# Optimization experiments

Measured on AMD Instinct MI355X. Metric: run time of the kernel, lower is better.

The kernel has to match this reference:

```python
import jax, jax.numpy as jnp
import numpy as np
from jax import lax

B, T, C, F_IN = 16, 128, 64, 128
H, FO = 4, 16          # GAT heads, out-features per head (gat_out)
HID = 32               # LSTM hidden (bidirectional -> 64)
NCLS = 3
TOPK, THR, TEMP = 2, 0.3, 1.5


def _layernorm(x, g, b, eps=1e-5):
    m = x.mean(-1, keepdims=True)
    v = ((x - m) ** 2).mean(-1, keepdims=True)
    return (x - m) / jnp.sqrt(v + eps) * g + b


def setup_inputs() -> dict:
    key = jax.random.key(0)
    ks = jax.random.split(key, 16)
    def lin(k, o, i):
        return jax.random.normal(k, (o, i), jnp.float32) / np.sqrt(i)
    return {
        "x": jax.random.uniform(ks[0], (B, T, C, F_IN), jnp.float32),
        "spec_w": jnp.ones((C, F_IN), jnp.float32),
        "gat_W": lin(ks[1], H * FO, F_IN),
        "gat_a": jax.random.normal(ks[2], (H, 2 * FO), jnp.float32),
        "gat_norm_g": jnp.ones((H * FO,), jnp.float32),
        "gat_norm_b": jnp.zeros((H * FO,), jnp.float32),
        "gat_res_W": lin(ks[3], H * FO, F_IN),
        "gat_res_b": jnp.zeros((H * FO,), jnp.float32),
        "lW_ih_f": lin(ks[4], 4 * HID, H * FO),
        "lW_hh_f": lin(ks[5], 4 * HID, HID),
        "lb_ih_f": jnp.zeros((4 * HID,), jnp.float32),
        "lb_hh_f": jnp.zeros((4 * HID,), jnp.float32),
        "lW_ih_b": lin(ks[6], 4 * HID, H * FO),
        "lW_hh_b": lin(ks[7], 4 * HID, HID),
        "lb_ih_b": jnp.zeros((4 * HID,), jnp.float32),
        "lb_hh_b": jnp.zeros((4 * HID,), jnp.float32),
        "ta_W": lin(ks[8], 2 * HID, 2 * HID),
        "ta_b": jnp.zeros((2 * HID,), jnp.float32),
        "ta_v": lin(ks[9], 1, 2 * HID),
        "cp_W": lin(ks[10], 1, 2 * HID),
        "cp_b": jnp.zeros((1,), jnp.float32),
        "norm_g": jnp.ones((2 * HID,), jnp.float32),
        "norm_b": jnp.zeros((2 * HID,), jnp.float32),
        "fc1_W": lin(ks[11], 32, 2 * HID),
        "fc1_b": jnp.zeros((32,), jnp.float32),
        "fc2_W": lin(ks[12], NCLS, 32),
        "fc2_b": jnp.zeros((NCLS,), jnp.float32),
    }


def _lstm(xs, Wih, Whh, bih, bhh):
    # xs: [T, N, in] -> [T, N, HID]; PyTorch gate order i,f,g,o
    N = xs.shape[1]
    def step(carry, xt):
        h, c = carry
        z = xt @ Wih.T + h @ Whh.T + bih + bhh
        i, f, g, o = jnp.split(z, 4, axis=-1)
        c = jax.nn.sigmoid(f) * c + jax.nn.sigmoid(i) * jnp.tanh(g)
        h = jax.nn.sigmoid(o) * jnp.tanh(c)
        return (h, c), h
    init = (jnp.zeros((N, HID), xs.dtype), jnp.zeros((N, HID), xs.dtype))
    return lax.scan(step, init, xs)[1]


def reference(x, spec_w, gat_W, gat_a, gat_norm_g, gat_norm_b, gat_res_W, gat_res_b,
              lW_ih_f, lW_hh_f, lb_ih_f, lb_hh_f, lW_ih_b, lW_hh_b, lb_ih_b, lb_hh_b,
              ta_W, ta_b, ta_v, cp_W, cp_b, norm_g, norm_b,
              fc1_W, fc1_b, fc2_W, fc2_b):
    # --- spectral weighting ---
    x = x * jax.nn.sigmoid(spec_w)                               # [B,T,C,F]
    # --- per-sample correlation graph (vectorized over B,T) ---
    Hn = x / (jnp.linalg.norm(x, axis=-1, keepdims=True) + 1e-8)
    A = jnp.einsum('btcf,btdf->bcd', Hn, Hn) / T                 # mean over T
    A = 0.5 * (A + jnp.swapaxes(A, 1, 2))
    # --- sparsify: per-row top-(k+1), threshold, off-diagonal, symmetrize ---
    _, idx = lax.top_k(A, TOPK + 1)                              # [B,C,k+1]
    topm = jax.nn.one_hot(idx, C).sum(axis=2) > 0                # [B,C,C]
    eye = jnp.eye(C, dtype=bool)
    keep = topm & (A > THR) & ~eye
    keep = keep | jnp.swapaxes(keep, 1, 2)
    A_s = jnp.where(keep, A, 0.0)                                # [B,C,C]
    # --- multi-head GAT, vectorized over all timesteps ---
    Wh = jnp.einsum('btcf,gf->btcg', x, gat_W).reshape(B, T, C, H, FO)
    ei = jnp.einsum('btchf,hf->btch', Wh, gat_a[:, :FO])
    ej = jnp.einsum('btchf,hf->btch', Wh, gat_a[:, FO:])
    e = ei[:, :, :, None, :] + ej[:, :, None, :, :]              # [B,T,C,C,H]
    e = jnp.where(e > 0, e, 0.2 * e)                             # LeakyReLU(0.2)
    mask = (A_s > 0) | eye                                       # [B,C,C]
    e = jnp.where(mask[:, None, :, :, None], e, -1e9)
    An = A_s / (A_s.sum(-1, keepdims=True) + 1e-8)
    e = e + An[:, None, :, :, None]
    alpha = jax.nn.softmax(e / TEMP, axis=3)                     # over j
    Hout = jnp.einsum('btijh,btjhf->btihf', alpha, Wh).reshape(B, T, C, H * FO)
    res = jnp.einsum('btcf,gf->btcg', x, gat_res_W) + gat_res_b
    g = jax.nn.relu(_layernorm(Hout + res, gat_norm_g, gat_norm_b))  # [B,T,C,64]
    # --- BiLSTM over T for each (faithful torch .view on [B,T,C,Fp]) ---
    seq = g.reshape(B * C, T, H * FO)
    xs = jnp.swapaxes(seq, 0, 1)                                 # [T,N,64]
    hf = _lstm(xs, lW_ih_f, lW_hh_f, lb_ih_f, lb_hh_f)
    hb = _lstm(xs[::-1], lW_ih_b, lW_hh_b, lb_ih_b, lb_hh_b)[::-1]
    h = jnp.swapaxes(jnp.concatenate([hf, hb], -1), 0, 1)        # [N,T,64]
    # --- temporal attention ---
    sc = (jnp.tanh(h @ ta_W.T + ta_b) @ ta_v.T)[..., 0]          # [N,T]
    al = jax.nn.softmax(sc / TEMP, axis=1)
    hp = (h * al[..., None]).sum(1)                              # [N,64]
    # --- channel attention pooling ---
    xc = hp.reshape(B, C, 2 * HID)
    w = jax.nn.softmax(xc @ cp_W.T + cp_b, axis=1)               # [B,C,1]
    pooled = (xc * w).sum(1)                                     # [B,64]
    pooled = _layernorm(pooled, norm_g, norm_b)
    hid = jax.nn.relu(pooled @ fc1_W.T + fc1_b)
    return hid @ fc2_W.T + fc2_b                                 # [B,3]
```

## Files before the change

### kernel.cpp

```cpp
#include <hip/hip_runtime.h>
#include <math.h>

#define BB 16
#define TT 128
#define CC 64
#define FF 128

static constexpr float INV_TEMP = 1.0f / 1.5f;

static constexpr size_t OFF_WTT   = 8192;
static constexpr size_t OFF_RTT   = 16384;
static constexpr size_t OFF_TAWT  = 24576;
static constexpr size_t OFF_AN    = 28672;
static constexpr size_t OFF_A     = 94208;
static constexpr size_t OFF_G     = 1208320;
static constexpr size_t OFF_H     = 9596928;
static constexpr size_t OFF_HP    = 17985536;
static constexpr size_t OFF_WIHT  = 18051072;
static constexpr size_t OFF_ZX    = 18067456;
static constexpr size_t OFF_XW    = OFF_ZX;
static constexpr size_t OFF_WHS   = OFF_ZX + 16777216;
static constexpr size_t OFF_RS    = OFF_ZX + 25165824;
static constexpr size_t OFF_APART = OFF_WHS;

__global__ __launch_bounds__(256) void k_xw(const float* __restrict__ x,
                                            const float* __restrict__ spec_w,
                                            float* __restrict__ xw) {
    const size_t i4 = (size_t)blockIdx.x * 256 + threadIdx.x;
    const float4 xv = ((const float4*)x)[i4];
    const int cf = (int)((i4 * 4) & 8191);
    const float4 wv = *(const float4*)(spec_w + cf);
    float4 o;
    o.x = xv.x / (1.f + __expf(-wv.x));
    o.y = xv.y / (1.f + __expf(-wv.y));
    o.z = xv.z / (1.f + __expf(-wv.z));
    o.w = xv.w / (1.f + __expf(-wv.w));
    ((float4*)xw)[i4] = o;
}

__global__ __launch_bounds__(256) void k_prep(const float* __restrict__ gat_W,
                                              const float* __restrict__ gat_rW,
                                              const float* __restrict__ ta_W,
                                              const float* __restrict__ Wihf,
                                              const float* __restrict__ Wihb,
                                              float* __restrict__ ws) {
    int i = blockIdx.x * 256 + threadIdx.x;
    if (i < 8192) {
        int k = i >> 6, g = i & 63;
        ws[OFF_WTT + i] = gat_W[g * 128 + k];
    } else if (i < 16384) {
        int j = i - 8192; int k = j >> 6, g = j & 63;
        ws[OFF_RTT + j] = gat_rW[g * 128 + k];
    } else if (i < 20480) {
        int j = i - 16384; int v = j >> 6, u = j & 63;
        ws[OFF_TAWT + j] = ta_W[u * 64 + v];
    } else if (i < 36864) {
        int j = i - 20480;
        int dir = j >> 13, rem = j & 8191, k = rem >> 7, gg = rem & 127;
        const float* W = dir ? Wihb : Wihf;
        ws[OFF_WIHT + j] = W[gg * 64 + k];
    }
}

__global__ __launch_bounds__(256) void k_corr(const float* __restrict__ xw,
                                              float* __restrict__ ws) {
    __shared__ __align__(16) float tile[64 * 132];
    __shared__ float rn[64];
    const int ch = blockIdx.x, b = blockIdx.y, tid = threadIdx.x;
    const int lane = tid & 63, wave = tid >> 6;
    const int c0 = wave * 16 + ((lane >> 4) << 2);
    const int d0 = (lane & 15) << 2;
    float acc[4][4];
#pragma unroll
    for (int a = 0; a < 4; ++a)
#pragma unroll
        for (int e = 0; e < 4; ++e) acc[a][e] = 0.f;

    for (int t8 = 0; t8 < 2; ++t8) {
        const int t = ch * 2 + t8;
        __syncthreads();
        const float4* __restrict__ xp4 = (const float4*)(xw + ((size_t)(b * TT + t)) * CC * FF);
        for (int i4 = tid; i4 < 2048; i4 += 256) {
            const int row = i4 >> 5, col4 = i4 & 31;
            *(float4*)&tile[row * 132 + col4 * 4] = xp4[i4];
        }
        __syncthreads();
        {
            const int row = tid >> 2, part = tid & 3;
            const float4* tr = (const float4*)(tile + row * 132 + part * 32);
            float s = 0.f;
#pragma unroll
            for (int q = 0; q < 8; ++q) {
                const float4 v = tr[q];
                s += v.x * v.x + v.y * v.y + v.z * v.z + v.w * v.w;
            }
            s += __shfl_xor(s, 1); s += __shfl_xor(s, 2);
            if (part == 0) rn[row] = 1.f / (sqrtf(s) + 1e-8f);
        }
        __syncthreads();
        float dot[4][4];
#pragma unroll
        for (int a = 0; a < 4; ++a)
#pragma unroll
            for (int e = 0; e < 4; ++e) dot[a][e] = 0.f;
        for (int f4 = 0; f4 < 32; ++f4) {
            float4 xc4[4], xd4[4];
#pragma unroll
            for (int a = 0; a < 4; ++a) xc4[a] = *(const float4*)&tile[(c0 + a) * 132 + f4 * 4];
#pragma unroll
            for (int e = 0; e < 4; ++e) xd4[e] = *(const float4*)&tile[(d0 + e) * 132 + f4 * 4];
#pragma unroll
            for (int a = 0; a < 4; ++a)
#pragma unroll
                for (int e = 0; e < 4; ++e)
                    dot[a][e] += xc4[a].x * xd4[e].x + xc4[a].y * xd4[e].y +
                                 xc4[a].z * xd4[e].z + xc4[a].w * xd4[e].w;
        }
#pragma unroll
        for (int a = 0; a < 4; ++a) {
            const float ra = rn[c0 + a];
#pragma unroll
            for (int e = 0; e < 4; ++e) acc[a][e] += ra * rn[d0 + e] * dot[a][e];
        }
    }
    float* __restrict__ Ap = ws + OFF_APART + ((size_t)(b * 64 + ch)) * 4096;
#pragma unroll
    for (int a = 0; a < 4; ++a)
#pragma unroll
        for (int e = 0; e < 4; ++e) Ap[(c0 + a) * 64 + d0 + e] = acc[a][e];
}

__global__ __launch_bounds__(256) void k_reduceA(float* __restrict__ ws) {
    int i = blockIdx.x * 256 + threadIdx.x;
    int b = i >> 12, e = i & 4095;
    const float* Ap = ws + OFF_APART + (size_t)b * 64 * 4096;
    float s = 0.f;
#pragma unroll 8
    for (int ch = 0; ch < 64; ++ch) s += Ap[ch * 4096 + e];
    ws[OFF_A + i] = s * (1.f / 128.f);
}

__global__ __launch_bounds__(64) void k_sparsify(float* __restrict__ ws) {
    __shared__ float As[64 * 65];
    __shared__ unsigned char kp[64 * 64];
    const int b = blockIdx.x, tid = threadIdx.x;
    const float* Ag = ws + OFF_A + (size_t)b * 4096;
    for (int m = 0; m < 64; ++m) As[m * 65 + tid] = Ag[m * 64 + tid];
    __syncthreads();
    const int c = tid;
    int s0 = -1, s1 = -1, s2 = -1;
    for (int p = 0; p < 3; ++p) {
        float best = -1e30f; int bi = -1;
        for (int d = 0; d < 64; ++d) {
            if (d == s0 || d == s1) continue;
            float v = As[c * 65 + d];
            if (v > best) { best = v; bi = d; }
        }
        if (p == 0) s0 = bi; else if (p == 1) s1 = bi; else s2 = bi;
    }
    for (int d = 0; d < 64; ++d) {
        float v = As[c * 65 + d];
        kp[c * 64 + d] = (unsigned char)(((d == s0) | (d == s1) | (d == s2)) &&
                                         (v > 0.3f) && (d != c));
    }
    __syncthreads();
    float rs = 0.f;
    for (int d = 0; d < 64; ++d) {
        bool k2 = kp[c * 64 + d] || kp[d * 64 + c];
        rs += k2 ? As[c * 65 + d] : 0.f;
    }
    const float inv = 1.f / (rs + 1e-8f);
    float* An = ws + OFF_AN + (size_t)b * 4096;
    for (int d = 0; d < 64; ++d) {
        bool k2 = kp[c * 64 + d] || kp[d * 64 + c];
        An[c * 64 + d] = k2 ? As[c * 65 + d] * inv : 0.f;
    }
}

__global__ __launch_bounds__(256) void k_wh(const float* __restrict__ xw,
                                            const float* __restrict__ wt,
                                            const float* __restrict__ rt,
                                            float* __restrict__ whs,
                                            float* __restrict__ rs,
                                            const float* __restrict__ res_b) {
    __shared__ __align__(16) float tile[64 * 132];
    const int bt = blockIdx.x, tid = threadIdx.x;
    const float4* __restrict__ xp4 = (const float4*)(xw + (size_t)bt * 8192);
    for (int i4 = tid; i4 < 2048; i4 += 256) {
        const int row = i4 >> 5, col4 = i4 & 31;
        *(float4*)&tile[row * 132 + col4 * 4] = xp4[i4];
    }
    __syncthreads();
    const int tx = tid & 31, ty = tid >> 5;
    const int mat = tx >> 4, cx = tx & 15;
    const int r0 = ty * 8, c0 = cx * 4;
    const float* __restrict__ wbase = mat ? rt : wt;
    float acc[8][4];
#pragma unroll
    for (int i = 0; i < 8; ++i)
#pragma unroll
        for (int j = 0; j < 4; ++j) acc[i][j] = 0.f;
    for (int k4 = 0; k4 < 32; ++k4) {
        float xs[8][4];
#pragma unroll
        for (int i = 0; i < 8; ++i) {
            const float4 v = *(const float4*)&tile[(r0 + i) * 132 + k4 * 4];
            xs[i][0] = v.x; xs[i][1] = v.y; xs[i][2] = v.z; xs[i][3] = v.w;
        }
#pragma unroll
        for (int kk = 0; kk < 4; ++kk) {
            const float4 wv = *(const float4*)(wbase + (k4 * 4 + kk) * 64 + c0);
#pragma unroll
            for (int i = 0; i < 8; ++i) {
                acc[i][0] += xs[i][kk] * wv.x;
                acc[i][1] += xs[i][kk] * wv.y;
                acc[i][2] += xs[i][kk] * wv.z;
                acc[i][3] += xs[i][kk] * wv.w;
            }
        }
    }
    if (mat == 0) {
        float* __restrict__ op = whs + (size_t)bt * 4096;
#pragma unroll
        for (int i = 0; i < 8; ++i) {
            float4 o; o.x = acc[i][0]; o.y = acc[i][1]; o.z = acc[i][2]; o.w = acc[i][3];
            *(float4*)(op + (r0 + i) * 64 + c0) = o;
        }
    } else {
        const float4 rb = *(const float4*)(res_b + c0);
        float* __restrict__ op = rs + (size_t)bt * 4096;
#pragma unroll
        for (int i = 0; i < 8; ++i) {
            float4 o; o.x = acc[i][0] + rb.x; o.y = acc[i][1] + rb.y;
            o.z = acc[i][2] + rb.z; o.w = acc[i][3] + rb.w;
            *(float4*)(op + (r0 + i) * 64 + c0) = o;
        }
    }
}

__global__ __launch_bounds__(256) void k_att(const float* __restrict__ ws,
                                             const float* __restrict__ whs,
                                             const float* __restrict__ rs,
                                             float* __restrict__ g,
                                             const float* __restrict__ gat_a,
                                             const float* __restrict__ ln_g,
                                             const float* __restrict__ ln_b) {
    __shared__ __align__(16) float sWh[64 * 68];
    __shared__ float sAn[64 * 65];
    __shared__ float sEjT[256];
    __shared__ float sStat[64 * 8];
    const int t = blockIdx.x, b = blockIdx.y, tid = threadIdx.x;
    const size_t bt = (size_t)(b * TT + t);
    const float4* __restrict__ wh4 = (const float4*)(whs + bt * 4096);
    for (int i4 = tid; i4 < 1024; i4 += 256) {
        const int row = i4 >> 4, c4 = i4 & 15;
        *(float4*)&sWh[row * 68 + c4 * 4] = wh4[i4];
    }
    const float* __restrict__ ang = ws + OFF_AN + (size_t)b * 4096;
    for (int i = tid; i < 4096; i += 256) sAn[(i >> 6) * 65 + (i & 63)] = ang[i];
    __syncthreads();

    const int ia = tid & 63, ha = tid >> 6;
    float eiv = 0.f, ejv = 0.f;
    {
        const float* __restrict__ whrow = sWh + ia * 68 + ha * 16;
        const float* __restrict__ aip = gat_a + ha * 32;
#pragma unroll
        for (int q = 0; q < 16; ++q) {
            const float w = whrow[q];
            eiv += w * aip[q];
            ejv += w * aip[16 + q];
        }
    }
    sEjT[ha * 64 + ia] = ejv;
    __syncthreads();

    float ao[16];
#pragma unroll
    for (int f = 0; f < 16; ++f) ao[f] = 0.f;
    float sum = 0.f;
    const float* __restrict__ anrow = sAn + ia * 65;
    const float* __restrict__ ejrow = sEjT + ha * 64;
#pragma unroll 4
    for (int j = 0; j < 64; ++j) {
        const float s = eiv + ejrow[j];
        const float l = s > 0.f ? s : 0.2f * s;
        const float anv = anrow[j];
        const float z = (anv != 0.f || j == ia) ? (l + anv) : -1e9f;
        const float p = __expf(z * INV_TEMP);
        sum += p;
        const float* __restrict__ wj = sWh + j * 68 + ha * 16;
        const float4 w0 = *(const float4*)(wj);
        const float4 w1 = *(const float4*)(wj + 4);
        const float4 w2 = *(const float4*)(wj + 8);
        const float4 w3 = *(const float4*)(wj + 12);
        ao[0]  += p * w0.x; ao[1]  += p * w0.y; ao[2]  += p * w0.z; ao[3]  += p * w0.w;
        ao[4]  += p * w1.x; ao[5]  += p * w1.y; ao[6]  += p * w1.z; ao[7]  += p * w1.w;
        ao[8]  += p * w2.x; ao[9]  += p * w2.y; ao[10] += p * w2.z; ao[11] += p * w2.w;
        ao[12] += p * w3.x; ao[13] += p * w3.y; ao[14] += p * w3.z; ao[15] += p * w3.w;
    }
    const float inv = 1.f / sum;
    float val[16];
    float s1 = 0.f, s2 = 0.f;
    const float* __restrict__ rsp = rs + bt * 4096 + ia * 64 + ha * 16;
#pragma unroll
    for (int q = 0; q < 4; ++q) {
        const float4 rv = *(const float4*)(rsp + q * 4);
        val[q * 4 + 0] = ao[q * 4 + 0] * inv + rv.x;
        val[q * 4 + 1] = ao[q * 4 + 1] * inv + rv.y;
        val[q * 4 + 2] = ao[q * 4 + 2] * inv + rv.z;
        val[q * 4 + 3] = ao[q * 4 + 3] * inv + rv.w;
    }
#pragma unroll
    for (int f = 0; f < 16; ++f) { s1 += val[f]; s2 += val[f] * val[f]; }
    sStat[ia * 8 + ha] = s1;
    sStat[ia * 8 + 4 + ha] = s2;
    __syncthreads();
    const float tsum = sStat[ia * 8 + 0] + sStat[ia * 8 + 1] + sStat[ia * 8 + 2] + sStat[ia * 8 + 3];
    const float tsq  = sStat[ia * 8 + 4] + sStat[ia * 8 + 5] + sStat[ia * 8 + 6] + sStat[ia * 8 + 7];
    const float mean = tsum * (1.f / 64.f);
    const float var = tsq * (1.f / 64.f) - mean * mean;
    const float rstd = rsqrtf(var + 1e-5f);
    float* __restrict__ gout = g + bt * 4096 + ia * 64 + ha * 16;
#pragma unroll
    for (int q = 0; q < 4; ++q) {
        const float4 gm = *(const float4*)(ln_g + ha * 16 + q * 4);
        const float4 bt4 = *(const float4*)(ln_b + ha * 16 + q * 4);
        float4 o;
        o.x = fmaxf((val[q * 4 + 0] - mean) * rstd * gm.x + bt4.x, 0.f);
        o.y = fmaxf((val[q * 4 + 1] - mean) * rstd * gm.y + bt4.y, 0.f);
        o.z = fmaxf((val[q * 4 + 2] - mean) * rstd * gm.z + bt4.z, 0.f);
        o.w = fmaxf((val[q * 4 + 3] - mean) * rstd * gm.w + bt4.w, 0.f);
        *(float4*)(gout + q * 4) = o;
    }
}

__global__ __launch_bounds__(256) void k_zx(const float* __restrict__ gbuf,
                                            const float* __restrict__ ws,
                                            float* __restrict__ zx,
                                            const float* __restrict__ bihf, const float* __restrict__ bhhf,
                                            const float* __restrict__ bihb, const float* __restrict__ bhhb) {
    __shared__ __align__(16) float gS[128 * 68];
    const int mt2 = blockIdx.x, dir = blockIdx.y, tid = threadIdx.x;
    const float4* __restrict__ gsrc4 = (const float4*)(gbuf + (size_t)mt2 * 8192);
    for (int i4 = tid; i4 < 2048; i4 += 256) {
        const int row = i4 >> 4, c4 = i4 & 15;
        *(float4*)&gS[row * 68 + c4 * 4] = gsrc4[i4];
    }
// ... 4 lines not shown
    float acc[8][8];
#pragma unroll
    for (int i = 0; i < 8; ++i)
#pragma unroll
        for (int j = 0; j < 8; ++j) acc[i][j] = 0.f;
    for (int k4 = 0; k4 < 16; ++k4) {
        float xs[8][4];
#pragma unroll
        for (int i = 0; i < 8; ++i) {
            const float4 v = *(const float4*)&gS[(ty + 16 * i) * 68 + k4 * 4];
            xs[i][0] = v.x; xs[i][1] = v.y; xs[i][2] = v.z; xs[i][3] = v.w;
        }
#pragma unroll
        for (int kk = 0; kk < 4; ++kk) {
            const float4 w0 = *(const float4*)(wT + (k4 * 4 + kk) * 128 + c0);
            const float4 w1 = *(const float4*)(wT + (k4 * 4 + kk) * 128 + c0 + 4);
#pragma unroll
            for (int i = 0; i < 8; ++i) {
                const float xv = xs[i][kk];
                acc[i][0] += xv * w0.x; acc[i][1] += xv * w0.y;
                acc[i][2] += xv * w0.z; acc[i][3] += xv * w0.w;
                acc[i][4] += xv * w1.x; acc[i][5] += xv * w1.y;
                acc[i][6] += xv * w1.z; acc[i][7] += xv * w1.w;
            }
        }
    }
    const float* bi = dir ? bihb : bihf;
    const float* bh = dir ? bhhb : bhhf;
    float bsum[8];
    {
        const float4 b0 = *(const float4*)(bi + c0), b1 = *(const float4*)(bi + c0 + 4);
        const float4 h0 = *(const float4*)(bh + c0), h1 = *(const float4*)(bh + c0 + 4);
        bsum[0] = b0.x + h0.x; bsum[1] = b0.y + h0.y; bsum[2] = b0.z + h0.z; bsum[3] = b0.w + h0.w;
        bsum[4] = b1.x + h1.x; bsum[5] = b1.y + h1.y; bsum[6] = b1.z + h1.z; bsum[7] = b1.w + h1.w;
    }
    float* __restrict__ zrow = zx + (size_t)dir * 16777216 + (size_t)mt2 * 16384;
#pragma unroll
    for (int i = 0; i < 8; ++i) {
        const int r = ty + 16 * i;
        float4 o0, o1;
        o0.x = acc[i][0] + bsum[0]; o0.y = acc[i][1] + bsum[1];
        o0.z = acc[i][2] + bsum[2]; o0.w = acc[i][3] + bsum[3];
        o1.x = acc[i][4] + bsum[4]; o1.y = acc[i][5] + bsum[5];
        o1.z = acc[i][6] + bsum[6]; o1.w = acc[i][7] + bsum[7];
        *(float4*)&zrow[r * 128 + c0] = o0;
        *(float4*)&zrow[r * 128 + c0 + 4] = o1;
    }
}

__device__ __forceinline__ float rl(float v, int l) {
    return __int_as_float(__builtin_amdgcn_readlane(__float_as_int(v), l));
}

__global__ __launch_bounds__(64, 1) void k_lstm2(const float* __restrict__ zx,
                                                 float* __restrict__ hbuf,
                                                 const float* __restrict__ Whhf,
                                                 const float* __restrict__ Whhb) {
    const int n = blockIdx.x, dir = blockIdx.y, r = threadIdx.x;
    const bool lo = (r < 32);
    const float* __restrict__ Whh = dir ? Whhb : Whhf;
    const float4* W4 = (const float4*)Whh;
    const float4 wa0 = W4[r * 8 + 0], wa1 = W4[r * 8 + 1], wa2 = W4[r * 8 + 2], wa3 = W4[r * 8 + 3];
    const float4 wa4 = W4[r * 8 + 4], wa5 = W4[r * 8 + 5], wa6 = W4[r * 8 + 6], wa7 = W4[r * 8 + 7];
    const float4 wb0 = W4[(r + 64) * 8 + 0], wb1 = W4[(r + 64) * 8 + 1];
    const float4 wb2 = W4[(r + 64) * 8 + 2], wb3 = W4[(r + 64) * 8 + 3];
    const float4 wb4 = W4[(r + 64) * 8 + 4], wb5 = W4[(r + 64) * 8 + 5];
    const float4 wb6 = W4[(r + 64) * 8 + 6], wb7 = W4[(r + 64) * 8 + 7];
    const float* __restrict__ zxp = zx + (size_t)dir * 16777216 + (size_t)n * 16384;
    float* __restrict__ hout = hbuf + (size_t)n * 8192 + dir * 32 + r;
    float hv = 0.f, cv = 0.f;

#define SADDR(S_) (zxp + (size_t)(dir ? 127 - (S_) : (S_)) * 128)
#define DOT4(Q) {                                                           \
        const float h0 = rl(hv, 4 * Q + 0), h1 = rl(hv, 4 * Q + 1);         \
        const float h2 = rl(hv, 4 * Q + 2), h3 = rl(hv, 4 * Q + 3);         \
        a0 += h0 * wa##Q.x; b0 += h0 * wb##Q.x;                             \
        a1 += h1 * wa##Q.y; b1 += h1 * wb##Q.y;                             \
        a0 += h2 * wa##Q.z; b0 += h2 * wb##Q.z;                             \
        a1 += h3 * wa##Q.w; b1 += h3 * wb##Q.w;                             \
    }
#define STEP(S_, ZA, ZB) {                                                  \
        float a0 = (ZA), a1 = 0.f, b0 = (ZB), b1 = 0.f;                     \
        DOT4(0) DOT4(1) DOT4(2) DOT4(3) DOT4(4) DOT4(5) DOT4(6) DOT4(7)    \
        const float zi = a0 + a1, zg = b0 + b1;                             \
        const float eA = __expf(-zi);                                       \
        const float sA = 1.f / (1.f + eA);                                  \
        const float eB = __expf(lo ? -2.f * zg : -zg);                      \
        const float vB = lo ? (2.f / (1.f + eB) - 1.f) : (1.f / (1.f + eB));\
        const float fv = __shfl_xor(sA, 32);                                \
        const float ox = __shfl_xor(vB, 32);                                \
        cv = fv * cv + sA * vB;                                             \
        const float eC = __expf(-2.f * cv);                                 \
        const float tc = 2.f / (1.f + eC) - 1.f;                            \
        hv = ox * tc;                                                       \
        const int s__ = dir ? 127 - (S_) : (S_);                            \
        if (lo) hout[s__ * 64] = hv;                                        \
    }

    const float* p0 = SADDR(0);
    const float* p1 = SADDR(1);
    float zA0 = p0[r], zB0 = p0[r + 64];
    float zA1 = p1[r], zB1 = p1[r + 64];
    for (int s2 = 0; s2 < 64; ++s2) {
        int sp = 2 * s2 + 2; if (sp > 126) sp = 126;
        const float* pn0 = SADDR(sp);
        const float* pn1 = SADDR(sp + 1);
        const float nA0 = pn0[r], nB0 = pn0[r + 64];
        const float nA1 = pn1[r], nB1 = pn1[r + 64];
        STEP(2 * s2, zA0, zB0);
        STEP(2 * s2 + 1, zA1, zB1);
        zA0 = nA0; zB0 = nB0; zA1 = nA1; zB1 = nB1;
    }
#undef STEP
#undef DOT4
#undef SADDR
}

__global__ __launch_bounds__(256) void k_ta(float* __restrict__ ws,
                                            const float* __restrict__ tab,
                                            const float* __restrict__ tav) {
    __shared__ __align__(16) float hL[128 * 68];
    __shared__ float scL[128];
    __shared__ float sRed[4];
    __shared__ float sPart[256];
    const int n = blockIdx.x, tid = threadIdx.x, lane = tid & 63, wave = tid >> 6;
    const float4* __restrict__ hsrc4 = (const float4*)(ws + OFF_H + (size_t)n * 8192);
    for (int i4 = tid; i4 < 2048; i4 += 256) {
        const int row = i4 >> 4, c4 = i4 & 15;
        *(float4*)&hL[row * 68 + c4 * 4] = hsrc4[i4];
    }
    __syncthreads();
    const int ty8 = lane >> 3, ux = lane & 7;
    const int t0 = wave * 32 + ty8, u0 = ux * 8;
    const float* __restrict__ twt = ws + OFF_TAWT;
    float tb[8], tv[8];
    *(float4*)&tb[0] = *(const float4*)(tab + u0);
    *(float4*)&tb[4] = *(const float4*)(tab + u0 + 4);
    *(float4*)&tv[0] = *(const float4*)(tav + u0);
    *(float4*)&tv[4] = *(const float4*)(tav + u0 + 4);
    float a[4][8];
#pragma unroll
    for (int i = 0; i < 4; ++i)
#pragma unroll
        for (int j = 0; j < 8; ++j) a[i][j] = 0.f;
    for (int v4 = 0; v4 < 16; ++v4) {
        float xs[4][4];
#pragma unroll
        for (int i = 0; i < 4; ++i) {
            const float4 v = *(const float4*)&hL[(t0 + 8 * i) * 68 + v4 * 4];
            xs[i][0] = v.x; xs[i][1] = v.y; xs[i][2] = v.z; xs[i][3] = v.w;
        }
#pragma unroll
        for (int kk = 0; kk < 4; ++kk) {
            const float4 w0 = *(const float4*)(twt + (v4 * 4 + kk) * 64 + u0);
            const float4 w1 = *(const float4*)(twt + (v4 * 4 + kk) * 64 + u0 + 4);
#pragma unroll
            for (int i = 0; i < 4; ++i) {
                const float xv = xs[i][kk];
                a[i][0] += xv * w0.x; a[i][1] += xv * w0.y;
                a[i][2] += xv * w0.z; a[i][3] += xv * w0.w;
                a[i][4] += xv * w1.x; a[i][5] += xv * w1.y;
                a[i][6] += xv * w1.z; a[i][7] += xv * w1.w;
            }
        }
    }
#pragma unroll
    for (int i = 0; i < 4; ++i) {
// ... 66 lines not shown
    float vv = d * d;
    for (int o = 1; o < 64; o <<= 1) vv += __shfl_xor(vv, o);
    const float pl = d * rsqrtf(vv * (1.f / 64.f) + 1e-5f) * ng[tid] + nb[tid];
    plL[tid] = pl;
    __syncthreads();
    if (tid < 32) {
        float h1 = f1b[tid];
        for (int j = 0; j < 64; ++j) h1 += plL[j] * f1W[tid * 64 + j];
        h1L[tid] = fmaxf(h1, 0.f);
    }
    __syncthreads();
    if (tid < 3) {
        float o = f2b[tid];
        for (int uu = 0; uu < 32; ++uu) o += h1L[uu] * f2W[tid * 32 + uu];
        out[b * 3 + tid] = o;
    }
}

extern "C" void kernel_launch(void* const* d_in, const int* in_sizes, int n_in,
                              void* d_out, int out_size, void* d_ws, size_t ws_size,
                              hipStream_t stream) {
    (void)in_sizes; (void)n_in; (void)out_size; (void)ws_size;
    const float* x      = (const float*)d_in[0];
    const float* spec_w = (const float*)d_in[1];
    const float* gat_W  = (const float*)d_in[2];
    const float* gat_a  = (const float*)d_in[3];
    const float* gat_ng = (const float*)d_in[4];
    const float* gat_nb = (const float*)d_in[5];
    const float* gat_rW = (const float*)d_in[6];
    const float* gat_rb = (const float*)d_in[7];
    const float* Wihf   = (const float*)d_in[8];
    const float* Whhf   = (const float*)d_in[9];
    const float* bihf   = (const float*)d_in[10];
    const float* bhhf   = (const float*)d_in[11];
    const float* Wihb   = (const float*)d_in[12];
    const float* Whhb   = (const float*)d_in[13];
    const float* bihb   = (const float*)d_in[14];
    const float* bhhb   = (const float*)d_in[15];
    const float* ta_W   = (const float*)d_in[16];
    const float* ta_b   = (const float*)d_in[17];
    const float* ta_v   = (const float*)d_in[18];
    const float* cp_W   = (const float*)d_in[19];
    const float* cp_b   = (const float*)d_in[20];
    const float* norm_g = (const float*)d_in[21];
    const float* norm_b = (const float*)d_in[22];
    const float* fc1_W  = (const float*)d_in[23];
    const float* fc1_b  = (const float*)d_in[24];
    const float* fc2_W  = (const float*)d_in[25];
    const float* fc2_b  = (const float*)d_in[26];
    float* ws  = (float*)d_ws;
    float* out = (float*)d_out;

    hipLaunchKernelGGL(k_prep, dim3(144), dim3(256), 0, stream, gat_W, gat_rW, ta_W, Wihf, Wihb, ws);
    hipLaunchKernelGGL(k_xw, dim3(16384), dim3(256), 0, stream, x, spec_w, ws + OFF_XW);
    hipLaunchKernelGGL(k_corr, dim3(64, 16), dim3(256), 0, stream, ws + OFF_XW, ws);
    hipLaunchKernelGGL(k_reduceA, dim3(256), dim3(256), 0, stream, ws);
    hipLaunchKernelGGL(k_sparsify, dim3(16), dim3(64), 0, stream, ws);
    hipLaunchKernelGGL(k_wh, dim3(2048), dim3(256), 0, stream,
                       ws + OFF_XW, ws + OFF_WTT, ws + OFF_RTT,
                       ws + OFF_WHS, ws + OFF_RS, gat_rb);
    hipLaunchKernelGGL(k_att, dim3(128, 16), dim3(256), 0, stream,
                       ws, ws + OFF_WHS, ws + OFF_RS, ws + OFF_G,
                       gat_a, gat_ng, gat_nb);
    hipLaunchKernelGGL(k_zx, dim3(1024, 2), dim3(256), 0, stream,
                       ws + OFF_G, ws, ws + OFF_ZX, bihf, bhhf, bihb, bhhb);
    hipLaunchKernelGGL(k_lstm2, dim3(1024, 2), dim3(64), 0, stream,
                       ws + OFF_ZX, ws + OFF_H, Whhf, Whhb);
    hipLaunchKernelGGL(k_ta, dim3(1024), dim3(256), 0, stream, ws, ta_b, ta_v);
    hipLaunchKernelGGL(k_final, dim3(16), dim3(64), 0, stream, ws, cp_W, cp_b,
                       norm_g, norm_b, fc1_W, fc1_b, fc2_W, fc2_b, out);
}
```

Before: 428.0 us.

## Fuse spectral sigmoid gating into consumers and move half of LSTM weights to LDS

Drops the standalone k_xw pass, which wrote the 64 MB gated copy of x, and applies the sigmoid(spec_w) scaling inline while k_corr and k_wh load tiles straight from x. This removes one full read and write of the large input, at the cost of recomputing the exp in each consumer. It also rewrites the LSTM recurrence kernel to keep the second half of each lane's W_hh rows in XOR-swizzled shared memory, reading them with LDS loads every step. The asm barrier on the indices stops the compiler from hoisting those loads back into registers. The aim is lower register pressure, in exchange for extra LDS traffic on the serial critical path.

```diff
diff --git a/kernel.cpp b/kernel.cpp
--- a/kernel.cpp
+++ b/kernel.cpp
@@ -18,25 +18,9 @@
 static constexpr size_t OFF_HP    = 17985536;
 static constexpr size_t OFF_WIHT  = 18051072;
 static constexpr size_t OFF_ZX    = 18067456;
-static constexpr size_t OFF_XW    = OFF_ZX;
 static constexpr size_t OFF_WHS   = OFF_ZX + 16777216;
 static constexpr size_t OFF_RS    = OFF_ZX + 25165824;
 static constexpr size_t OFF_APART = OFF_WHS;
-
-__global__ __launch_bounds__(256) void k_xw(const float* __restrict__ x,
-                                            const float* __restrict__ spec_w,
-                                            float* __restrict__ xw) {
-    const size_t i4 = (size_t)blockIdx.x * 256 + threadIdx.x;
-    const float4 xv = ((const float4*)x)[i4];
-    const int cf = (int)((i4 * 4) & 8191);
-    const float4 wv = *(const float4*)(spec_w + cf);
-    float4 o;
-    o.x = xv.x / (1.f + __expf(-wv.x));
-    o.y = xv.y / (1.f + __expf(-wv.y));
-    o.z = xv.z / (1.f + __expf(-wv.z));
-    o.w = xv.w / (1.f + __expf(-wv.w));
-    ((float4*)xw)[i4] = o;
-}
 
 __global__ __launch_bounds__(256) void k_prep(const float* __restrict__ gat_W,
                                               const float* __restrict__ gat_rW,
@@ -62,7 +46,17 @@
     }
 }
 
-__global__ __launch_bounds__(256) void k_corr(const float* __restrict__ xw,
+__device__ __forceinline__ float4 sigmul4(const float4 xv, const float4 wv) {
+    float4 o;
+    o.x = xv.x / (1.f + __expf(-wv.x));
+    o.y = xv.y / (1.f + __expf(-wv.y));
+    o.z = xv.z / (1.f + __expf(-wv.z));
+    o.w = xv.w / (1.f + __expf(-wv.w));
+    return o;
+}
+
+__global__ __launch_bounds__(256) void k_corr(const float* __restrict__ x,
+                                              const float* __restrict__ spec_w,
                                               float* __restrict__ ws) {
     __shared__ __align__(16) float tile[64 * 132];
     __shared__ float rn[64];
@@ -70,6 +64,7 @@
     const int lane = tid & 63, wave = tid >> 6;
     const int c0 = wave * 16 + ((lane >> 4) << 2);
     const int d0 = (lane & 15) << 2;
+    const float4* __restrict__ sg4 = (const float4*)spec_w;
     float acc[4][4];
 #pragma unroll
     for (int a = 0; a < 4; ++a)
@@ -79,10 +74,10 @@
     for (int t8 = 0; t8 < 2; ++t8) {
         const int t = ch * 2 + t8;
         __syncthreads();
-        const float4* __restrict__ xp4 = (const float4*)(xw + ((size_t)(b * TT + t)) * CC * FF);
+        const float4* __restrict__ xp4 = (const float4*)(x + ((size_t)(b * TT + t)) * CC * FF);
         for (int i4 = tid; i4 < 2048; i4 += 256) {
             const int row = i4 >> 5, col4 = i4 & 31;
-            *(float4*)&tile[row * 132 + col4 * 4] = xp4[i4];
+            *(float4*)&tile[row * 132 + col4 * 4] = sigmul4(xp4[i4], sg4[i4]);
         }
         __syncthreads();
         {
@@ -177,7 +172,8 @@
     }
 }
 
-__global__ __launch_bounds__(256) void k_wh(const float* __restrict__ xw,
+__global__ __launch_bounds__(256) void k_wh(const float* __restrict__ x,
+                                            const float* __restrict__ spec_w,
                                             const float* __restrict__ wt,
                                             const float* __restrict__ rt,
                                             float* __restrict__ whs,
@@ -185,10 +181,11 @@
                                             const float* __restrict__ res_b) {
     __shared__ __align__(16) float tile[64 * 132];
     const int bt = blockIdx.x, tid = threadIdx.x;
-    const float4* __restrict__ xp4 = (const float4*)(xw + (size_t)bt * 8192);
+    const float4* __restrict__ xp4 = (const float4*)(x + (size_t)bt * 8192);
+    const float4* __restrict__ sg4 = (const float4*)spec_w;
     for (int i4 = tid; i4 < 2048; i4 += 256) {
         const int row = i4 >> 5, col4 = i4 & 31;
-        *(float4*)&tile[row * 132 + col4 * 4] = xp4[i4];
+        *(float4*)&tile[row * 132 + col4 * 4] = sigmul4(xp4[i4], sg4[i4]);
     }
     __syncthreads();
     const int tx = tid & 31, ty = tid >> 5;
@@ -404,36 +401,49 @@
     return __int_as_float(__builtin_amdgcn_readlane(__float_as_int(v), l));
 }
 
-__global__ __launch_bounds__(64, 1) void k_lstm2(const float* __restrict__ zx,
+__global__ __launch_bounds__(64, 1) void k_lstm5(const float* __restrict__ zx,
                                                  float* __restrict__ hbuf,
                                                  const float* __restrict__ Whhf,
                                                  const float* __restrict__ Whhb) {
+    __shared__ __align__(16) float swb[2048];
     const int n = blockIdx.x, dir = blockIdx.y, r = threadIdx.x;
     const bool lo = (r < 32);
+    const int rx = r & 7;
     const float* __restrict__ Whh = dir ? Whhb : Whhf;
     const float4* W4 = (const float4*)Whh;
+    {
+        float4* sw = (float4*)swb;
+#pragma unroll
+        for (int q = 0; q < 8; ++q)
+            sw[r * 8 + (q ^ rx)] = W4[(64 + r) * 8 + q];
+    }
     const float4 wa0 = W4[r * 8 + 0], wa1 = W4[r * 8 + 1], wa2 = W4[r * 8 + 2], wa3 = W4[r * 8 + 3];
     const float4 wa4 = W4[r * 8 + 4], wa5 = W4[r * 8 + 5], wa6 = W4[r * 8 + 6], wa7 = W4[r * 8 + 7];
-    const float4 wb0 = W4[(r + 64) * 8 + 0], wb1 = W4[(r + 64) * 8 + 1];
-    const float4 wb2 = W4[(r + 64) * 8 + 2], wb3 = W4[(r + 64) * 8 + 3];
-    const float4 wb4 = W4[(r + 64) * 8 + 4], wb5 = W4[(r + 64) * 8 + 5];
-    const float4 wb6 = W4[(r + 64) * 8 + 6], wb7 = W4[(r + 64) * 8 + 7];
+    __syncthreads();
+    const float4* sw4 = (const float4*)swb;
+    int j0 = r * 8 + (0 ^ rx), j1 = r * 8 + (1 ^ rx), j2 = r * 8 + (2 ^ rx), j3 = r * 8 + (3 ^ rx);
+    int j4 = r * 8 + (4 ^ rx), j5 = r * 8 + (5 ^ rx), j6 = r * 8 + (6 ^ rx), j7 = r * 8 + (7 ^ rx);
     const float* __restrict__ zxp = zx + (size_t)dir * 16777216 + (size_t)n * 16384;
     float* __restrict__ hout = hbuf + (size_t)n * 8192 + dir * 32 + r;
     float hv = 0.f, cv = 0.f;
 
 #define SADDR(S_) (zxp + (size_t)(dir ? 127 - (S_) : (S_)) * 128)
-#define DOT4(Q) {                                                           \
+#define DOTQ(Q, U) {                                                        \
         const float h0 = rl(hv, 4 * Q + 0), h1 = rl(hv, 4 * Q + 1);         \
         const float h2 = rl(hv, 4 * Q + 2), h3 = rl(hv, 4 * Q + 3);         \
-        a0 += h0 * wa##Q.x; b0 += h0 * wb##Q.x;                             \
-        a1 += h1 * wa##Q.y; b1 += h1 * wb##Q.y;                             \
-        a0 += h2 * wa##Q.z; b0 += h2 * wb##Q.z;                             \
-        a1 += h3 * wa##Q.w; b1 += h3 * wb##Q.w;                             \
+        a0 += h0 * wa##Q.x; b0 += h0 * U.x;                                 \
+        a1 += h1 * wa##Q.y; b1 += h1 * U.y;                                 \
+        a0 += h2 * wa##Q.z; b0 += h2 * U.z;                                 \
+        a1 += h3 * wa##Q.w; b1 += h3 * U.w;                                 \
     }
 #define STEP(S_, ZA, ZB) {                                                  \
+        asm volatile("" : "+v"(j0), "+v"(j1), "+v"(j2), "+v"(j3),           \
+                          "+v"(j4), "+v"(j5), "+v"(j6), "+v"(j7));          \
+        const float4 u0 = sw4[j0], u1 = sw4[j1], u2 = sw4[j2], u3 = sw4[j3];\
+        const float4 u4 = sw4[j4], u5 = sw4[j5], u6 = sw4[j6], u7 = sw4[j7];\
         float a0 = (ZA), a1 = 0.f, b0 = (ZB), b1 = 0.f;                     \
-        DOT4(0) DOT4(1) DOT4(2) DOT4(3) DOT4(4) DOT4(5) DOT4(6) DOT4(7)    \
+        DOTQ(0, u0) DOTQ(1, u1) DOTQ(2, u2) DOTQ(3, u3)                     \
+        DOTQ(4, u4) DOTQ(5, u5) DOTQ(6, u6) DOTQ(7, u7)                     \
         const float zi = a0 + a1, zg = b0 + b1;                             \
         const float eA = __expf(-zi);                                       \
         const float sA = 1.f / (1.f + eA);                                  \
@@ -464,7 +474,7 @@
         zA0 = nA0; zB0 = nB0; zA1 = nA1; zB1 = nB1;
     }
 #undef STEP
-#undef DOT4
+#undef DOTQ
 #undef SADDR
 }
 
@@ -637,19 +647,18 @@
     float* out = (float*)d_out;
 
     hipLaunchKernelGGL(k_prep, dim3(144), dim3(256), 0, stream, gat_W, gat_rW, ta_W, Wihf, Wihb, ws);
-    hipLaunchKernelGGL(k_xw, dim3(16384), dim3(256), 0, stream, x, spec_w, ws + OFF_XW);
-    hipLaunchKernelGGL(k_corr, dim3(64, 16), dim3(256), 0, stream, ws + OFF_XW, ws);
+    hipLaunchKernelGGL(k_corr, dim3(64, 16), dim3(256), 0, stream, x, spec_w, ws);
     hipLaunchKernelGGL(k_reduceA, dim3(256), dim3(256), 0, stream, ws);
     hipLaunchKernelGGL(k_sparsify, dim3(16), dim3(64), 0, stream, ws);
     hipLaunchKernelGGL(k_wh, dim3(2048), dim3(256), 0, stream,
-                       ws + OFF_XW, ws + OFF_WTT, ws + OFF_RTT,
+                       x, spec_w, ws + OFF_WTT, ws + OFF_RTT,
                        ws + OFF_WHS, ws + OFF_RS, gat_rb);
     hipLaunchKernelGGL(k_att, dim3(128, 16), dim3(256), 0, stream,
                        ws, ws + OFF_WHS, ws + OFF_RS, ws + OFF_G,
                        gat_a, gat_ng, gat_nb);
     hipLaunchKernelGGL(k_zx, dim3(1024, 2), dim3(256), 0, stream,
                        ws + OFF_G, ws, ws + OFF_ZX, bihf, bhhf, bihb, bhhb);
-    hipLaunchKernelGGL(k_lstm2, dim3(1024, 2), dim3(64), 0, stream,
+    hipLaunchKernelGGL(k_lstm5, dim3(1024, 2), dim3(64), 0, stream,
                        ws + OFF_ZX, ws + OFF_H, Whhf, Whhb);
     hipLaunchKernelGGL(k_ta, dim3(1024), dim3(256), 0, stream, ws, ta_b, ta_v);
     hipLaunchKernelGGL(k_final, dim3(16), dim3(64), 0, stream, ws, cp_W, cp_b,
```

After: 419.8 us. Within noise of the previous version (-1.9%).

## Fuse spectral sigmoid weighting into corr and GAT projection loads, merge weight matrices

Applied to the files above, without the earlier changes.

Drops the standalone elementwise kernel that wrote a sigmoid-weighted copy of x (about 64MB) to the workspace. k_corr and k_wh now apply the sigmoid(spec_w) scaling while staging raw x tiles into shared memory. The GAT W and residual W transposes are packed into one 128-column matrix, so k_wh computes both products with a 4x8 register tile per thread instead of splitting threads by matrix. This removes a full write and re-read of the large activation tensor, at the cost of recomputing the exp in both consumers.

```diff
diff --git a/kernel.cpp b/kernel.cpp
--- a/kernel.cpp
+++ b/kernel.cpp
@@ -8,8 +8,7 @@
 
 static constexpr float INV_TEMP = 1.0f / 1.5f;
 
-static constexpr size_t OFF_WTT   = 8192;
-static constexpr size_t OFF_RTT   = 16384;
+static constexpr size_t OFF_WRT   = 8192;
 static constexpr size_t OFF_TAWT  = 24576;
 static constexpr size_t OFF_AN    = 28672;
 static constexpr size_t OFF_A     = 94208;
@@ -18,25 +17,9 @@
 static constexpr size_t OFF_HP    = 17985536;
 static constexpr size_t OFF_WIHT  = 18051072;
 static constexpr size_t OFF_ZX    = 18067456;
-static constexpr size_t OFF_XW    = OFF_ZX;
 static constexpr size_t OFF_WHS   = OFF_ZX + 16777216;
 static constexpr size_t OFF_RS    = OFF_ZX + 25165824;
 static constexpr size_t OFF_APART = OFF_WHS;
-
-__global__ __launch_bounds__(256) void k_xw(const float* __restrict__ x,
-                                            const float* __restrict__ spec_w,
-                                            float* __restrict__ xw) {
-    const size_t i4 = (size_t)blockIdx.x * 256 + threadIdx.x;
-    const float4 xv = ((const float4*)x)[i4];
-    const int cf = (int)((i4 * 4) & 8191);
-    const float4 wv = *(const float4*)(spec_w + cf);
-    float4 o;
-    o.x = xv.x / (1.f + __expf(-wv.x));
-    o.y = xv.y / (1.f + __expf(-wv.y));
-    o.z = xv.z / (1.f + __expf(-wv.z));
-    o.w = xv.w / (1.f + __expf(-wv.w));
-    ((float4*)xw)[i4] = o;
-}
 
 __global__ __launch_bounds__(256) void k_prep(const float* __restrict__ gat_W,
                                               const float* __restrict__ gat_rW,
@@ -45,12 +28,9 @@
                                               const float* __restrict__ Wihb,
                                               float* __restrict__ ws) {
     int i = blockIdx.x * 256 + threadIdx.x;
-    if (i < 8192) {
-        int k = i >> 6, g = i & 63;
-        ws[OFF_WTT + i] = gat_W[g * 128 + k];
-    } else if (i < 16384) {
-        int j = i - 8192; int k = j >> 6, g = j & 63;
-        ws[OFF_RTT + j] = gat_rW[g * 128 + k];
+    if (i < 16384) {
+        int k = i >> 7, g = i & 127;
+        ws[OFF_WRT + i] = (g < 64) ? gat_W[g * 128 + k] : gat_rW[(g - 64) * 128 + k];
     } else if (i < 20480) {
         int j = i - 16384; int v = j >> 6, u = j & 63;
         ws[OFF_TAWT + j] = ta_W[u * 64 + v];
@@ -62,7 +42,17 @@
     }
 }
 
-__global__ __launch_bounds__(256) void k_corr(const float* __restrict__ xw,
+__device__ __forceinline__ float4 sigmul4(const float4 xv, const float4 wv) {
+    float4 o;
+    o.x = xv.x / (1.f + __expf(-wv.x));
+    o.y = xv.y / (1.f + __expf(-wv.y));
+    o.z = xv.z / (1.f + __expf(-wv.z));
+    o.w = xv.w / (1.f + __expf(-wv.w));
+    return o;
+}
+
+__global__ __launch_bounds__(256) void k_corr(const float* __restrict__ x,
+                                              const float* __restrict__ spec_w,
                                               float* __restrict__ ws) {
     __shared__ __align__(16) float tile[64 * 132];
     __shared__ float rn[64];
@@ -70,6 +60,7 @@
     const int lane = tid & 63, wave = tid >> 6;
     const int c0 = wave * 16 + ((lane >> 4) << 2);
     const int d0 = (lane & 15) << 2;
+    const float4* __restrict__ sg4 = (const float4*)spec_w;
     float acc[4][4];
 #pragma unroll
     for (int a = 0; a < 4; ++a)
@@ -79,10 +70,10 @@
     for (int t8 = 0; t8 < 2; ++t8) {
         const int t = ch * 2 + t8;
         __syncthreads();
-        const float4* __restrict__ xp4 = (const float4*)(xw + ((size_t)(b * TT + t)) * CC * FF);
+        const float4* __restrict__ xp4 = (const float4*)(x + ((size_t)(b * TT + t)) * CC * FF);
         for (int i4 = tid; i4 < 2048; i4 += 256) {
             const int row = i4 >> 5, col4 = i4 & 31;
-            *(float4*)&tile[row * 132 + col4 * 4] = xp4[i4];
+            *(float4*)&tile[row * 132 + col4 * 4] = sigmul4(xp4[i4], sg4[i4]);
         }
         __syncthreads();
         {
@@ -177,63 +168,73 @@
     }
 }
 
-__global__ __launch_bounds__(256) void k_wh(const float* __restrict__ xw,
-                                            const float* __restrict__ wt,
-                                            const float* __restrict__ rt,
+__global__ __launch_bounds__(256) void k_wh(const float* __restrict__ x,
+                                            const float* __restrict__ spec_w,
+                                            const float* __restrict__ wrt,
                                             float* __restrict__ whs,
                                             float* __restrict__ rs,
                                             const float* __restrict__ res_b) {
     __shared__ __align__(16) float tile[64 * 132];
     const int bt = blockIdx.x, tid = threadIdx.x;
-    const float4* __restrict__ xp4 = (const float4*)(xw + (size_t)bt * 8192);
+    const float4* __restrict__ xp4 = (const float4*)(x + (size_t)bt * 8192);
+    const float4* __restrict__ sg4 = (const float4*)spec_w;
     for (int i4 = tid; i4 < 2048; i4 += 256) {
         const int row = i4 >> 5, col4 = i4 & 31;
-        *(float4*)&tile[row * 132 + col4 * 4] = xp4[i4];
-    }
-    __syncthreads();
-    const int tx = tid & 31, ty = tid >> 5;
-    const int mat = tx >> 4, cx = tx & 15;
-    const int r0 = ty * 8, c0 = cx * 4;
-    const float* __restrict__ wbase = mat ? rt : wt;
-    float acc[8][4];
-#pragma unroll
-    for (int i = 0; i < 8; ++i)
-#pragma unroll
-        for (int j = 0; j < 4; ++j) acc[i][j] = 0.f;
+        *(float4*)&tile[row * 132 + col4 * 4] = sigmul4(xp4[i4], sg4[i4]);
+    }
+    __syncthreads();
+    const int tx = tid & 15, ty = tid >> 4;
+    const int c0 = tx * 8, r0 = ty * 4;
+    float acc[4][8];
+#pragma unroll
+    for (int i = 0; i < 4; ++i)
+#pragma unroll
+        for (int j = 0; j < 8; ++j) acc[i][j] = 0.f;
     for (int k4 = 0; k4 < 32; ++k4) {
-        float xs[8][4];
-#pragma unroll
-        for (int i = 0; i < 8; ++i) {
+        float xs[4][4];
+#pragma unroll
+        for (int i = 0; i < 4; ++i) {
             const float4 v = *(const float4*)&tile[(r0 + i) * 132 + k4 * 4];
             xs[i][0] = v.x; xs[i][1] = v.y; xs[i][2] = v.z; xs[i][3] = v.w;
         }
 #pragma unroll
         for (int kk = 0; kk < 4; ++kk) {
-            const float4 wv = *(const float4*)(wbase + (k4 * 4 + kk) * 64 + c0);
-#pragma unroll
-            for (int i = 0; i < 8; ++i) {
-                acc[i][0] += xs[i][kk] * wv.x;
-                acc[i][1] += xs[i][kk] * wv.y;
-                acc[i][2] += xs[i][kk] * wv.z;
-                acc[i][3] += xs[i][kk] * wv.w;
+            const float4 w0 = *(const float4*)(wrt + (k4 * 4 + kk) * 128 + c0);
+            const float4 w1 = *(const float4*)(wrt + (k4 * 4 + kk) * 128 + c0 + 4);
+#pragma unroll
+            for (int i = 0; i < 4; ++i) {
+                const float xv = xs[i][kk];
+                acc[i][0] += xv * w0.x; acc[i][1] += xv * w0.y;
+                acc[i][2] += xv * w0.z; acc[i][3] += xv * w0.w;
+                acc[i][4] += xv * w1.x; acc[i][5] += xv * w1.y;
+                acc[i][6] += xv * w1.z; acc[i][7] += xv * w1.w;
             }
         }
     }
-    if (mat == 0) {
+    if (c0 < 64) {
         float* __restrict__ op = whs + (size_t)bt * 4096;
 #pragma unroll
-        for (int i = 0; i < 8; ++i) {
-            float4 o; o.x = acc[i][0]; o.y = acc[i][1]; o.z = acc[i][2]; o.w = acc[i][3];
-            *(float4*)(op + (r0 + i) * 64 + c0) = o;
+        for (int i = 0; i < 4; ++i) {
+            float4 o0, o1;
+            o0.x = acc[i][0]; o0.y = acc[i][1]; o0.z = acc[i][2]; o0.w = acc[i][3];
+            o1.x = acc[i][4]; o1.y = acc[i][5]; o1.z = acc[i][6]; o1.w = acc[i][7];
+            *(float4*)(op + (r0 + i) * 64 + c0) = o0;
+            *(float4*)(op + (r0 + i) * 64 + c0 + 4) = o1;
         }
     } else {
-        const float4 rb = *(const float4*)(res_b + c0);
+        const int cr = c0 - 64;
+        const float4 rb0 = *(const float4*)(res_b + cr);
+        const float4 rb1 = *(const float4*)(res_b + cr + 4);
         float* __restrict__ op = rs + (size_t)bt * 4096;
 #pragma unroll
-        for (int i = 0; i < 8; ++i) {
-            float4 o; o.x = acc[i][0] + rb.x; o.y = acc[i][1] + rb.y;
-            o.z = acc[i][2] + rb.z; o.w = acc[i][3] + rb.w;
-            *(float4*)(op + (r0 + i) * 64 + c0) = o;
+        for (int i = 0; i < 4; ++i) {
+            float4 o0, o1;
+            o0.x = acc[i][0] + rb0.x; o0.y = acc[i][1] + rb0.y;
+            o0.z = acc[i][2] + rb0.z; o0.w = acc[i][3] + rb0.w;
+            o1.x = acc[i][4] + rb1.x; o1.y = acc[i][5] + rb1.y;
+            o1.z = acc[i][6] + rb1.z; o1.w = acc[i][7] + rb1.w;
+            *(float4*)(op + (r0 + i) * 64 + cr) = o0;
+            *(float4*)(op + (r0 + i) * 64 + cr + 4) = o1;
         }
     }
 }
@@ -637,12 +638,11 @@
     float* out = (float*)d_out;
 
     hipLaunchKernelGGL(k_prep, dim3(144), dim3(256), 0, stream, gat_W, gat_rW, ta_W, Wihf, Wihb, ws);
-    hipLaunchKernelGGL(k_xw, dim3(16384), dim3(256), 0, stream, x, spec_w, ws + OFF_XW);
-    hipLaunchKernelGGL(k_corr, dim3(64, 16), dim3(256), 0, stream, ws + OFF_XW, ws);
+    hipLaunchKernelGGL(k_corr, dim3(64, 16), dim3(256), 0, stream, x, spec_w, ws);
     hipLaunchKernelGGL(k_reduceA, dim3(256), dim3(256), 0, stream, ws);
     hipLaunchKernelGGL(k_sparsify, dim3(16), dim3(64), 0, stream, ws);
     hipLaunchKernelGGL(k_wh, dim3(2048), dim3(256), 0, stream,
-                       ws + OFF_XW, ws + OFF_WTT, ws + OFF_RTT,
+                       x, spec_w, ws + OFF_WRT,
                        ws + OFF_WHS, ws + OFF_RS, gat_rb);
     hipLaunchKernelGGL(k_att, dim3(128, 16), dim3(256), 0, stream,
                        ws, ws + OFF_WHS, ws + OFF_RS, ws + OFF_G,
```

Result: no change. 431.8 us (+0.9%).

## Fuse spectral sigmoid gating into corr and wh loads, drop xw pass

Applied to the files above, without the earlier changes.

Removes the standalone k_xw kernel that wrote a gated copy of x (about 64 MB) to workspace. k_corr and k_wh now apply the sigmoid(spec_w) scaling while loading x tiles, which removes one full write and the re-reads of the 64 MB intermediate at the cost of recomputing the exp. The gat_W and residual weights are interleaved into one 128-wide transposed matrix. k_att stops staging Wh in shared memory and reads it straight from global, which saves LDS and a barrier but may add global or L2 traffic.

```diff
diff --git a/kernel.cpp b/kernel.cpp
--- a/kernel.cpp
+++ b/kernel.cpp
@@ -8,8 +8,7 @@
 
 static constexpr float INV_TEMP = 1.0f / 1.5f;
 
-static constexpr size_t OFF_WTT   = 8192;
-static constexpr size_t OFF_RTT   = 16384;
+static constexpr size_t OFF_WRT   = 8192;
 static constexpr size_t OFF_TAWT  = 24576;
 static constexpr size_t OFF_AN    = 28672;
 static constexpr size_t OFF_A     = 94208;
@@ -18,25 +17,9 @@
 static constexpr size_t OFF_HP    = 17985536;
 static constexpr size_t OFF_WIHT  = 18051072;
 static constexpr size_t OFF_ZX    = 18067456;
-static constexpr size_t OFF_XW    = OFF_ZX;
 static constexpr size_t OFF_WHS   = OFF_ZX + 16777216;
 static constexpr size_t OFF_RS    = OFF_ZX + 25165824;
 static constexpr size_t OFF_APART = OFF_WHS;
-
-__global__ __launch_bounds__(256) void k_xw(const float* __restrict__ x,
-                                            const float* __restrict__ spec_w,
-                                            float* __restrict__ xw) {
-    const size_t i4 = (size_t)blockIdx.x * 256 + threadIdx.x;
-    const float4 xv = ((const float4*)x)[i4];
-    const int cf = (int)((i4 * 4) & 8191);
-    const float4 wv = *(const float4*)(spec_w + cf);
-    float4 o;
-    o.x = xv.x / (1.f + __expf(-wv.x));
-    o.y = xv.y / (1.f + __expf(-wv.y));
-    o.z = xv.z / (1.f + __expf(-wv.z));
-    o.w = xv.w / (1.f + __expf(-wv.w));
-    ((float4*)xw)[i4] = o;
-}
 
 __global__ __launch_bounds__(256) void k_prep(const float* __restrict__ gat_W,
                                               const float* __restrict__ gat_rW,
@@ -45,12 +28,9 @@
                                               const float* __restrict__ Wihb,
                                               float* __restrict__ ws) {
     int i = blockIdx.x * 256 + threadIdx.x;
-    if (i < 8192) {
-        int k = i >> 6, g = i & 63;
-        ws[OFF_WTT + i] = gat_W[g * 128 + k];
-    } else if (i < 16384) {
-        int j = i - 8192; int k = j >> 6, g = j & 63;
-        ws[OFF_RTT + j] = gat_rW[g * 128 + k];
+    if (i < 16384) {
+        int k = i >> 7, g = i & 127;
+        ws[OFF_WRT + i] = (g < 64) ? gat_W[g * 128 + k] : gat_rW[(g - 64) * 128 + k];
     } else if (i < 20480) {
         int j = i - 16384; int v = j >> 6, u = j & 63;
         ws[OFF_TAWT + j] = ta_W[u * 64 + v];
@@ -62,7 +42,17 @@
     }
 }
 
-__global__ __launch_bounds__(256) void k_corr(const float* __restrict__ xw,
+__device__ __forceinline__ float4 sigmul4(const float4 xv, const float4 wv) {
+    float4 o;
+    o.x = xv.x / (1.f + __expf(-wv.x));
+    o.y = xv.y / (1.f + __expf(-wv.y));
+    o.z = xv.z / (1.f + __expf(-wv.z));
+    o.w = xv.w / (1.f + __expf(-wv.w));
+    return o;
+}
+
+__global__ __launch_bounds__(256) void k_corr(const float* __restrict__ x,
+                                              const float* __restrict__ spec_w,
                                               float* __restrict__ ws) {
     __shared__ __align__(16) float tile[64 * 132];
     __shared__ float rn[64];
@@ -70,6 +60,7 @@
     const int lane = tid & 63, wave = tid >> 6;
     const int c0 = wave * 16 + ((lane >> 4) << 2);
     const int d0 = (lane & 15) << 2;
+    const float4* __restrict__ sg4 = (const float4*)spec_w;
     float acc[4][4];
 #pragma unroll
     for (int a = 0; a < 4; ++a)
@@ -79,10 +70,10 @@
     for (int t8 = 0; t8 < 2; ++t8) {
         const int t = ch * 2 + t8;
         __syncthreads();
-        const float4* __restrict__ xp4 = (const float4*)(xw + ((size_t)(b * TT + t)) * CC * FF);
+        const float4* __restrict__ xp4 = (const float4*)(x + ((size_t)(b * TT + t)) * CC * FF);
         for (int i4 = tid; i4 < 2048; i4 += 256) {
             const int row = i4 >> 5, col4 = i4 & 31;
-            *(float4*)&tile[row * 132 + col4 * 4] = xp4[i4];
+            *(float4*)&tile[row * 132 + col4 * 4] = sigmul4(xp4[i4], sg4[i4]);
         }
         __syncthreads();
         {
@@ -177,24 +168,25 @@
     }
 }
 
-__global__ __launch_bounds__(256) void k_wh(const float* __restrict__ xw,
-                                            const float* __restrict__ wt,
-                                            const float* __restrict__ rt,
+__global__ __launch_bounds__(256) void k_wh(const float* __restrict__ x,
+                                            const float* __restrict__ spec_w,
+                                            const float* __restrict__ wrt,
                                             float* __restrict__ whs,
                                             float* __restrict__ rs,
                                             const float* __restrict__ res_b) {
     __shared__ __align__(16) float tile[64 * 132];
     const int bt = blockIdx.x, tid = threadIdx.x;
-    const float4* __restrict__ xp4 = (const float4*)(xw + (size_t)bt * 8192);
+    const float4* __restrict__ xp4 = (const float4*)(x + (size_t)bt * 8192);
+    const float4* __restrict__ sg4 = (const float4*)spec_w;
     for (int i4 = tid; i4 < 2048; i4 += 256) {
         const int row = i4 >> 5, col4 = i4 & 31;
-        *(float4*)&tile[row * 132 + col4 * 4] = xp4[i4];
+        *(float4*)&tile[row * 132 + col4 * 4] = sigmul4(xp4[i4], sg4[i4]);
     }
     __syncthreads();
     const int tx = tid & 31, ty = tid >> 5;
     const int mat = tx >> 4, cx = tx & 15;
     const int r0 = ty * 8, c0 = cx * 4;
-    const float* __restrict__ wbase = mat ? rt : wt;
+    const float* __restrict__ wbase = wrt + (mat ? 64 : 0);
     float acc[8][4];
 #pragma unroll
     for (int i = 0; i < 8; ++i)
@@ -209,7 +201,7 @@
         }
 #pragma unroll
         for (int kk = 0; kk < 4; ++kk) {
-            const float4 wv = *(const float4*)(wbase + (k4 * 4 + kk) * 64 + c0);
+            const float4 wv = *(const float4*)(wbase + (k4 * 4 + kk) * 128 + c0);
 #pragma unroll
             for (int i = 0; i < 8; ++i) {
                 acc[i][0] += xs[i][kk] * wv.x;
@@ -245,25 +237,19 @@
                                              const float* __restrict__ gat_a,
                                              const float* __restrict__ ln_g,
                                              const float* __restrict__ ln_b) {
-    __shared__ __align__(16) float sWh[64 * 68];
     __shared__ float sAn[64 * 65];
     __shared__ float sEjT[256];
     __shared__ float sStat[64 * 8];
     const int t = blockIdx.x, b = blockIdx.y, tid = threadIdx.x;
     const size_t bt = (size_t)(b * TT + t);
-    const float4* __restrict__ wh4 = (const float4*)(whs + bt * 4096);
-    for (int i4 = tid; i4 < 1024; i4 += 256) {
-        const int row = i4 >> 4, c4 = i4 & 15;
-        *(float4*)&sWh[row * 68 + c4 * 4] = wh4[i4];
-    }
+    const float* __restrict__ whb = whs + bt * 4096;
     const float* __restrict__ ang = ws + OFF_AN + (size_t)b * 4096;
     for (int i = tid; i < 4096; i += 256) sAn[(i >> 6) * 65 + (i & 63)] = ang[i];
-    __syncthreads();
 
     const int ia = tid & 63, ha = tid >> 6;
     float eiv = 0.f, ejv = 0.f;
     {
-        const float* __restrict__ whrow = sWh + ia * 68 + ha * 16;
+        const float* __restrict__ whrow = whb + ia * 64 + ha * 16;
         const float* __restrict__ aip = gat_a + ha * 32;
 #pragma unroll
         for (int q = 0; q < 16; ++q) {
@@ -281,6 +267,7 @@
     float sum = 0.f;
     const float* __restrict__ anrow = sAn + ia * 65;
     const float* __restrict__ ejrow = sEjT + ha * 64;
+    const float* __restrict__ whp = whb + ha * 16;
 #pragma unroll 4
     for (int j = 0; j < 64; ++j) {
         const float s = eiv + ejrow[j];
@@ -289,11 +276,10 @@
         const float z = (anv != 0.f || j == ia) ? (l + anv) : -1e9f;
         const float p = __expf(z * INV_TEMP);
         sum += p;
-        const float* __restrict__ wj = sWh + j * 68 + ha * 16;
-        const float4 w0 = *(const float4*)(wj);
-        const float4 w1 = *(const float4*)(wj + 4);
-        const float4 w2 = *(const float4*)(wj + 8);
-        const float4 w3 = *(const float4*)(wj + 12);
+        const float4 w0 = *(const float4*)(whp + j * 64);
+        const float4 w1 = *(const float4*)(whp + j * 64 + 4);
+        const float4 w2 = *(const float4*)(whp + j * 64 + 8);
+        const float4 w3 = *(const float4*)(whp + j * 64 + 12);
         ao[0]  += p * w0.x; ao[1]  += p * w0.y; ao[2]  += p * w0.z; ao[3]  += p * w0.w;
         ao[4]  += p * w1.x; ao[5]  += p * w1.y; ao[6]  += p * w1.z; ao[7]  += p * w1.w;
         ao[8]  += p * w2.x; ao[9]  += p * w2.y; ao[10] += p * w2.z; ao[11] += p * w2.w;
@@ -637,12 +623,11 @@
     float* out = (float*)d_out;
 
     hipLaunchKernelGGL(k_prep, dim3(144), dim3(256), 0, stream, gat_W, gat_rW, ta_W, Wihf, Wihb, ws);
-    hipLaunchKernelGGL(k_xw, dim3(16384), dim3(256), 0, stream, x, spec_w, ws + OFF_XW);
-    hipLaunchKernelGGL(k_corr, dim3(64, 16), dim3(256), 0, stream, ws + OFF_XW, ws);
+    hipLaunchKernelGGL(k_corr, dim3(64, 16), dim3(256), 0, stream, x, spec_w, ws);
     hipLaunchKernelGGL(k_reduceA, dim3(256), dim3(256), 0, stream, ws);
     hipLaunchKernelGGL(k_sparsify, dim3(16), dim3(64), 0, stream, ws);
     hipLaunchKernelGGL(k_wh, dim3(2048), dim3(256), 0, stream,
-                       ws + OFF_XW, ws + OFF_WTT, ws + OFF_RTT,
+                       x, spec_w, ws + OFF_WRT,
                        ws + OFF_WHS, ws + OFF_RS, gat_rb);
     hipLaunchKernelGGL(k_att, dim3(128, 16), dim3(256), 0, stream,
                        ws, ws + OFF_WHS, ws + OFF_RS, ws + OFF_G,
```

Result: slower. 457.2 us (+6.8%).
